# Kernel tuning notes

Hardware: AMD Instinct MI355X
Metric: run time of the kernel (lower is better)

Reference implementation:

```python
import jax, jax.numpy as jnp
import numpy as np

N_NODES = 100000
N_EDGES = 3200000
IN_C, HID_C, OUT_C = 128, 64, 64


def setup_inputs() -> dict:
    key = jax.random.key(0)
    k = jax.random.split(key, 6)
    x = jax.random.normal(k[0], (N_NODES, IN_C), dtype=jnp.float32)
    edge_index = jax.random.randint(k[1], (2, N_EDGES), 0, N_NODES, dtype=jnp.int64)
    edge_weight = jax.random.uniform(k[2], (N_EDGES,), dtype=jnp.float32)
    W1 = jax.random.normal(k[3], (IN_C, HID_C), dtype=jnp.float32) * (1.0 / np.sqrt(IN_C))
    b1 = jnp.zeros((HID_C,), dtype=jnp.float32)
    W2 = jax.random.normal(k[4], (HID_C, OUT_C), dtype=jnp.float32) * (1.0 / np.sqrt(HID_C))
    b2 = jnp.zeros((OUT_C,), dtype=jnp.float32)
    return {"x": x, "edge_index": edge_index, "edge_weight": edge_weight,
            "W1": W1, "b1": b1, "W2": W2, "b2": b2}


def _gcn_norm(edge_index, edge_weight, num_nodes, dtype):
    # PyG GCNConv default: add self-loops (weight 1), symmetric normalization
    loop = jnp.arange(num_nodes, dtype=edge_index.dtype)
    row = jnp.concatenate([edge_index[0], loop])  # sources
    col = jnp.concatenate([edge_index[1], loop])  # targets (aggregation dim)
    w = jnp.concatenate([edge_weight.astype(dtype), jnp.ones((num_nodes,), dtype)])
    deg = jax.ops.segment_sum(w, col, num_segments=num_nodes)
    deg_inv_sqrt = jnp.where(deg > 0, jax.lax.rsqrt(deg), jnp.zeros((), dtype))
    norm = deg_inv_sqrt[row] * w * deg_inv_sqrt[col]
    return row, col, norm


def _gcn_conv(h, row, col, norm, W, b, num_nodes):
    h = h @ W                      # [N, C_out]
    msg = h[row] * norm[:, None]   # gather over sources, scale by edge norm
    out = jax.ops.segment_sum(msg, col, num_segments=num_nodes)  # scatter-add to targets
    return out + b


def reference(x, edge_index, edge_weight, W1, b1, W2, b2):
    num_nodes = x.shape[0]
    row, col, norm = _gcn_norm(edge_index, edge_weight, num_nodes, x.dtype)
    h = _gcn_conv(x, row, col, norm, W1, b1, num_nodes)
    h = jax.nn.relu(h)
    return _gcn_conv(h, row, col, norm, W2, b2, num_nodes)
```

## Files before the change

kernel.cpp:

```cpp
#include <hip/hip_runtime.h>
#include <hip/hip_bf16.h>

#define N_NODES 100000
#define N_EDGES 3200000
#define IN_C 128
#define HID_C 64
#define OUT_C 64

#define NBUCKET 196
#define SC_EDGES 4096
#define SC_GRID 782
#define CAP 18432

struct EdgeRec { int s; float v; };

typedef float f32x2 __attribute__((ext_vector_type(2)));

__device__ __forceinline__ unsigned pack_bf16(float lo, float hi) {
    unsigned short l = __hip_bfloat16_raw(__float2bfloat16(lo)).x;
    unsigned short h = __hip_bfloat16_raw(__float2bfloat16(hi)).x;
    return ((unsigned)h << 16) | l;
}
__device__ __forceinline__ float bf_lo(unsigned u) {
    union { unsigned u; float f; } c; c.u = u << 16; return c.f;
}
__device__ __forceinline__ float bf_hi(unsigned u) {
    union { unsigned u; float f; } c; c.u = u & 0xffff0000u; return c.f;
}
__device__ __forceinline__ f32x2 bfp(unsigned u) {
    union { unsigned u; float f; } lo, hi;
    lo.u = u << 16; hi.u = u & 0xffff0000u;
    f32x2 r; r.x = lo.f; r.y = hi.f; return r;
}
__device__ __forceinline__ void pk_fma(f32x2& acc, f32x2 a, f32x2 w) {
    asm("v_pk_fma_f32 %0, %1, %2, %0" : "+v"(acc) : "v"(a), "v"(w));
}
__device__ __forceinline__ void edge_acc(f32x2* acc2, uint4 u, float w) {
    f32x2 wv; wv.x = w; wv.y = w;
    pk_fma(acc2[0], bfp(u.x), wv);
    pk_fma(acc2[1], bfp(u.y), wv);
    pk_fma(acc2[2], bfp(u.z), wv);
    pk_fma(acc2[3], bfp(u.w), wv);
}

__global__ __launch_bounds__(256) void scatter_coarse(const int* __restrict__ ei,
                                                      const float* __restrict__ ew,
                                                      int* __restrict__ gcursor,
                                                      uint2* __restrict__ tmp) {
    __shared__ int hist[256];
    __shared__ int scan[256];
    __shared__ int lcur[256];
    __shared__ int adj[256];
    __shared__ uint2 rec[SC_EDGES];
    __shared__ unsigned char bk[SC_EDGES];
    int tid = threadIdx.x;
    hist[tid] = 0;
    __syncthreads();
    int base = blockIdx.x * SC_EDGES;
    unsigned ys[16];
    float    ws[16];
    int      bs[16];
    for (int i = 0; i < 16; ++i) {
        int e = base + i * 256 + tid;
        if (e < N_EDGES) {
            int t = ei[N_EDGES + e];
            bs[i] = t >> 9;
            ys[i] = (unsigned)ei[e] | ((unsigned)(t & 511) << 17);
            ws[i] = ew[e];
            atomicAdd(&hist[bs[i]], 1);
        } else bs[i] = -1;
    }
    __syncthreads();
    int v = hist[tid];
    scan[tid] = v;
    __syncthreads();
    for (int off = 1; off < 256; off <<= 1) {
        int t = scan[tid];
        int add = (tid >= off) ? scan[tid - off] : 0;
        __syncthreads();
        scan[tid] = t + add;
        __syncthreads();
    }
    int excl = scan[tid] - v;
    int gb = (v > 0) ? atomicAdd(&gcursor[tid], v) : 0;
    lcur[tid] = excl;
    adj[tid] = tid * CAP + gb - excl;
    __syncthreads();
    for (int i = 0; i < 16; ++i) {
        if (bs[i] >= 0) {
            int j = atomicAdd(&lcur[bs[i]], 1);
            rec[j] = make_uint2(__float_as_uint(ws[i]), ys[i]);
            bk[j] = (unsigned char)bs[i];
        }
    }
    __syncthreads();
    int count = N_EDGES - base;
    if (count > SC_EDGES) count = SC_EDGES;
    for (int j = tid; j < count; j += 256) {
        int b = bk[j];
        tmp[adj[b] + j] = rec[j];
    }
}

__global__ __launch_bounds__(256) void bucket_scan(const int* __restrict__ gcnt,
                                                   int* __restrict__ start) {
    __shared__ int s[256];
    int tid = threadIdx.x;
    int v = gcnt[tid];
    s[tid] = v;
    __syncthreads();
    for (int off = 1; off < 256; off <<= 1) {
        int t = s[tid];
        int add = (tid >= off) ? s[tid - off] : 0;
        __syncthreads();
        s[tid] = t + add;
        __syncthreads();
    }
    start[tid] = s[tid] - v;
    if (tid == 255) start[256] = s[255];
}

__global__ __launch_bounds__(512) void fine_sort(const int* __restrict__ start,
                                                 const uint2* __restrict__ tmpPad,
                                                 int* __restrict__ rowptr,
                                                 float* __restrict__ dis,
                                                 EdgeRec* __restrict__ ed) {
    __shared__ int   cnt[512];
    __shared__ float wdeg[512];
    __shared__ int   s[512];
    int tid = threadIdx.x;
    int nodeBase = blockIdx.x << 9;
    int bb = start[blockIdx.x];
    int nEdge = start[blockIdx.x + 1] - bb;
    const uint2* tb = tmpPad + (size_t)blockIdx.x * CAP;
    cnt[tid] = 0;
    wdeg[tid] = 0.f;
    __syncthreads();
    for (int e = tid; e < nEdge; e += 512) {
        uint2 r = tb[e];
        int l = (r.y >> 17) & 511;
        atomicAdd(&cnt[l], 1);
        atomicAdd(&wdeg[l], __uint_as_float(r.x));
    }
    __syncthreads();
    int v = cnt[tid];
    s[tid] = v;
    __syncthreads();
    for (int off = 1; off < 512; off <<= 1) {
        int t = s[tid];
        int add = (tid >= off) ? s[tid - off] : 0;
        __syncthreads();
        s[tid] = t + add;
        __syncthreads();
    }
    int excl = s[tid] - v;
    int node = nodeBase + tid;
    if (node < N_NODES) {
        rowptr[node] = bb + excl;
        dis[node] = rsqrtf(wdeg[tid] + 1.0f);
    }
    if (node == N_NODES) rowptr[N_NODES] = N_EDGES;
    cnt[tid] = excl;
    __syncthreads();
    for (int e = tid; e < nEdge; e += 512) {
        uint2 r = tb[e];
        int l = (r.y >> 17) & 511;
        int p = atomicAdd(&cnt[l], 1);
        EdgeRec o;
        o.s = (int)(r.y & 0x1FFFFu);
        o.v = __uint_as_float(r.x);
        ed[bb + p] = o;
    }
}

__global__ __launch_bounds__(256) void mm1_kernel(const float* __restrict__ x,
                                                  const float* __restrict__ W,
                                                  const float* __restrict__ dis,
                                                  unsigned* __restrict__ h) {
    __shared__ __align__(16) float xs[16][IN_C];
    __shared__ __align__(16) float wsm[IN_C][HID_C];
    int tid = threadIdx.x;
    {
        float4*       wd = (float4*)&wsm[0][0];
        const float4* wsrc = (const float4*)W;
        for (int i = tid; i < IN_C * HID_C / 4; i += 256) wd[i] = wsrc[i];
        float4*       xd = (float4*)&xs[0][0];
        const float4* xsrc = (const float4*)(x + (size_t)blockIdx.x * 16 * IN_C);
        for (int i = tid; i < 16 * IN_C / 4; i += 256) xd[i] = xsrc[i];
    }
    int rowBase = blockIdx.x * 16;
    __syncthreads();
    int c = tid & 63, rg = tid >> 6;
    const float4* xr0 = (const float4*)&xs[rg * 4 + 0][0];
    const float4* xr1 = (const float4*)&xs[rg * 4 + 1][0];
    const float4* xr2 = (const float4*)&xs[rg * 4 + 2][0];
    const float4* xr3 = (const float4*)&xs[rg * 4 + 3][0];
    float a0 = 0.f, a1 = 0.f, a2 = 0.f, a3 = 0.f;
    #pragma unroll 4
    for (int k4 = 0; k4 < IN_C / 4; ++k4) {
        float4 x0 = xr0[k4], x1 = xr1[k4], x2 = xr2[k4], x3 = xr3[k4];
        float w0 = wsm[4 * k4 + 0][c];
        float w1 = wsm[4 * k4 + 1][c];
        float w2 = wsm[4 * k4 + 2][c];
        float w3 = wsm[4 * k4 + 3][c];
        a0 += x0.x * w0 + x0.y * w1 + x0.z * w2 + x0.w * w3;
        a1 += x1.x * w0 + x1.y * w1 + x1.z * w2 + x1.w * w3;
        a2 += x2.x * w0 + x2.y * w1 + x2.z * w2 + x2.w * w3;
        a3 += x3.x * w0 + x3.y * w1 + x3.z * w2 + x3.w * w3;
    }
    a0 *= dis[rowBase + rg * 4 + 0];
    a1 *= dis[rowBase + rg * 4 + 1];
    a2 *= dis[rowBase + rg * 4 + 2];
    a3 *= dis[rowBase + rg * 4 + 3];
    float o0 = __shfl_xor(a0, 1, 64);
    float o1 = __shfl_xor(a1, 1, 64);
    float o2 = __shfl_xor(a2, 1, 64);
    float o3 = __shfl_xor(a3, 1, 64);
    if ((c & 1) == 0) {
        int ci = c >> 1;
        h[(rowBase + rg * 4 + 0) * 32 + ci] = pack_bf16(a0, o0);
        h[(rowBase + rg * 4 + 1) * 32 + ci] = pack_bf16(a1, o1);
        h[(rowBase + rg * 4 + 2) * 32 + ci] = pack_bf16(a2, o2);
        h[(rowBase + rg * 4 + 3) * 32 + ci] = pack_bf16(a3, o3);
    }
}

__global__ __launch_bounds__(256) void mm2_kernel(const float* __restrict__ a,
                                                  const float* __restrict__ W,
                                                  const float* __restrict__ dis,
                                                  unsigned* __restrict__ h) {
    __shared__ __align__(16) float as[16][HID_C];
    __shared__ __align__(16) float wsm[HID_C][OUT_C];
    int tid = threadIdx.x;
    {
        float4*       wd = (float4*)&wsm[0][0];
        const float4* wsrc = (const float4*)W;
        for (int i = tid; i < HID_C * OUT_C / 4; i += 256) wd[i] = wsrc[i];
        float4*       ad = (float4*)&as[0][0];
        const float4* asrc = (const float4*)(a + (size_t)blockIdx.x * 16 * HID_C);
        for (int i = tid; i < 16 * HID_C / 4; i += 256) ad[i] = asrc[i];
    }
    int rowBase = blockIdx.x * 16;
    __syncthreads();
    int c = tid & 63, rg = tid >> 6;
    const float4* xr0 = (const float4*)&as[rg * 4 + 0][0];
    const float4* xr1 = (const float4*)&as[rg * 4 + 1][0];
    const float4* xr2 = (const float4*)&as[rg * 4 + 2][0];
    const float4* xr3 = (const float4*)&as[rg * 4 + 3][0];
    float a0 = 0.f, a1 = 0.f, a2 = 0.f, a3 = 0.f;
    #pragma unroll 4
    for (int k4 = 0; k4 < HID_C / 4; ++k4) {
        float4 x0 = xr0[k4], x1 = xr1[k4], x2 = xr2[k4], x3 = xr3[k4];
        float w0 = wsm[4 * k4 + 0][c];
        float w1 = wsm[4 * k4 + 1][c];
        float w2 = wsm[4 * k4 + 2][c];
        float w3 = wsm[4 * k4 + 3][c];
        a0 += x0.x * w0 + x0.y * w1 + x0.z * w2 + x0.w * w3;
        a1 += x1.x * w0 + x1.y * w1 + x1.z * w2 + x1.w * w3;
        a2 += x2.x * w0 + x2.y * w1 + x2.z * w2 + x2.w * w3;
        a3 += x3.x * w0 + x3.y * w1 + x3.z * w2 + x3.w * w3;
    }
    a0 *= dis[rowBase + rg * 4 + 0];
    a1 *= dis[rowBase + rg * 4 + 1];
    a2 *= dis[rowBase + rg * 4 + 2];
    a3 *= dis[rowBase + rg * 4 + 3];
    float o0 = __shfl_xor(a0, 1, 64);
    float o1 = __shfl_xor(a1, 1, 64);
    float o2 = __shfl_xor(a2, 1, 64);
    float o3 = __shfl_xor(a3, 1, 64);
    if ((c & 1) == 0) {
        int ci = c >> 1;
        h[(rowBase + rg * 4 + 0) * 32 + ci] = pack_bf16(a0, o0);
        h[(rowBase + rg * 4 + 1) * 32 + ci] = pack_bf16(a1, o1);
        h[(rowBase + rg * 4 + 2) * 32 + ci] = pack_bf16(a2, o2);
        h[(rowBase + rg * 4 + 3) * 32 + ci] = pack_bf16(a3, o3);
    }
}

__global__ __launch_bounds__(256, 8) void agg_kernel(const int* __restrict__ rowptr,
                                                     const EdgeRec* __restrict__ ed,
                                                     const unsigned* __restrict__ h,
                                                     const float* __restrict__ dis,
                                                     const float* __restrict__ b,
                                                     float* __restrict__ out,
                                                     int relu) {
    int node = blockIdx.x * 4 + (threadIdx.x >> 6);
    int lane = threadIdx.x & 63;
    int g = lane >> 3;
    int cl = lane & 7;
    int beg = rowptr[node];
    int end = rowptr[node + 1];
    const uint4* h16 = (const uint4*)h;
    const char*  hb  = (const char*)h + (size_t)cl * 16;
    float d  = dis[node];
    uint4 us = h16[(size_t)node * 8 + cl];
    f32x2 acc2[4];
    acc2[0] = 0.f; acc2[1] = 0.f; acc2[2] = 0.f; acc2[3] = 0.f;
    int n = end - beg;
    int nb = (n + 31) >> 5;
    int nm1 = n - 1;
    uint2 q0, q1, q2, q3;
    if (nb > 0) {
        q0 = *(const uint2*)(ed + beg + min(g,      nm1));
        q1 = *(const uint2*)(ed + beg + min(g + 8,  nm1));
        q2 = *(const uint2*)(ed + beg + min(g + 16, nm1));
        q3 = *(const uint2*)(ed + beg + min(g + 24, nm1));
        for (int bt = 0; bt < nb; ++bt) {
            int ob = (bt << 5) + g;
            float w0 = (ob      < n) ? __uint_as_float(q0.y) : 0.f;
            float w1 = (ob + 8  < n) ? __uint_as_float(q1.y) : 0.f;
            float w2 = (ob + 16 < n) ? __uint_as_float(q2.y) : 0.f;
            float w3 = (ob + 24 < n) ? __uint_as_float(q3.y) : 0.f;
            uint4 u0 = *(const uint4*)(hb + ((size_t)(unsigned)q0.x << 7));
            uint4 u1 = *(const uint4*)(hb + ((size_t)(unsigned)q1.x << 7));
            uint4 u2 = *(const uint4*)(hb + ((size_t)(unsigned)q2.x << 7));
            uint4 u3 = *(const uint4*)(hb + ((size_t)(unsigned)q3.x << 7));
            if (bt + 1 < nb) {
                int on = ob + 32;
                q0 = *(const uint2*)(ed + beg + min(on,      nm1));
                q1 = *(const uint2*)(ed + beg + min(on + 8,  nm1));
                q2 = *(const uint2*)(ed + beg + min(on + 16, nm1));
                q3 = *(const uint2*)(ed + beg + min(on + 24, nm1));
            }
            edge_acc(acc2, u0, w0);
            edge_acc(acc2, u1, w1);
            edge_acc(acc2, u2, w2);
            edge_acc(acc2, u3, w3);
        }
    }
    float acc[8] = { acc2[0].x, acc2[0].y, acc2[1].x, acc2[1].y,
                     acc2[2].x, acc2[2].y, acc2[3].x, acc2[3].y };
    #pragma unroll
    for (int kk = 0; kk < 8; ++kk) {
        acc[kk] += __shfl_xor(acc[kk], 8, 64);
        acc[kk] += __shfl_xor(acc[kk], 16, 64);
        acc[kk] += __shfl_xor(acc[kk], 32, 64);
    }
    if (g == 0) {
        float hs[8] = { bf_lo(us.x), bf_hi(us.x), bf_lo(us.y), bf_hi(us.y),
                        bf_lo(us.z), bf_hi(us.z), bf_lo(us.w), bf_hi(us.w) };
        const float4* b4 = (const float4*)b;
        float4 bv0 = b4[cl * 2], bv1 = b4[cl * 2 + 1];
        float4 v0, v1;
        v0.x = d * (acc[0] + hs[0]) + bv0.x;
        v0.y = d * (acc[1] + hs[1]) + bv0.y;
        v0.z = d * (acc[2] + hs[2]) + bv0.z;
        v0.w = d * (acc[3] + hs[3]) + bv0.w;
        v1.x = d * (acc[4] + hs[4]) + bv1.x;
        v1.y = d * (acc[5] + hs[5]) + bv1.y;
        v1.z = d * (acc[6] + hs[6]) + bv1.z;
        v1.w = d * (acc[7] + hs[7]) + bv1.w;
        if (relu) {
            v0.x = fmaxf(v0.x, 0.f); v0.y = fmaxf(v0.y, 0.f);
            v0.z = fmaxf(v0.z, 0.f); v0.w = fmaxf(v0.w, 0.f);
            v1.x = fmaxf(v1.x, 0.f); v1.y = fmaxf(v1.y, 0.f);
            v1.z = fmaxf(v1.z, 0.f); v1.w = fmaxf(v1.w, 0.f);
        }
        float4* o4 = (float4*)out;
        o4[node * 16 + cl * 2]     = v0;
        o4[node * 16 + cl * 2 + 1] = v1;
    }
}

extern "C" void kernel_launch(void* const* d_in, const int* in_sizes, int n_in,
                              void* d_out, int out_size, void* d_ws, size_t ws_size,
                              hipStream_t stream) {
    const float* x  = (const float*)d_in[0];
    const int*   ei = (const int*)d_in[1];
    const float* ew = (const float*)d_in[2];
    const float* W1 = (const float*)d_in[3];
    const float* b1 = (const float*)d_in[4];
    const float* W2 = (const float*)d_in[5];
    const float* b2 = (const float*)d_in[6];
    float* out = (float*)d_out;

    char* p = (char*)d_ws;
    auto carve = [&](size_t bytes) { char* r = p; p += (bytes + 255) & ~(size_t)255; return r; };
    float*    dis     = (float*)carve(N_NODES * 4);
    int*      rowptr  = (int*)carve((N_NODES + 1) * 4);
    int*      start   = (int*)carve(257 * 4);
    int*      gcursor = (int*)carve(256 * 4);
    EdgeRec*  ed      = (EdgeRec*)carve((size_t)N_EDGES * 8);
    size_t    r2sz    = (size_t)NBUCKET * CAP * 8;
    size_t    hasz    = (size_t)N_NODES * 64 * 6;
    char*     r2      = carve(r2sz > hasz ? r2sz : hasz);
    uint2*    tmpPad  = (uint2*)r2;
    unsigned* h       = (unsigned*)r2;
    float*    a       = (float*)(r2 + (size_t)N_NODES * 64 * 2);

    hipMemsetAsync(gcursor, 0, 256 * sizeof(int), stream);
    scatter_coarse<<<SC_GRID, 256, 0, stream>>>(ei, ew, gcursor, tmpPad);
    bucket_scan<<<1, 256, 0, stream>>>(gcursor, start);
    fine_sort<<<NBUCKET, 512, 0, stream>>>(start, tmpPad, rowptr, dis, ed);

    mm1_kernel<<<N_NODES / 16, 256, 0, stream>>>(x, W1, dis, h);
    agg_kernel<<<N_NODES / 4, 256, 0, stream>>>(rowptr, ed, h, dis, b1, a, 1);

    mm2_kernel<<<N_NODES / 16, 256, 0, stream>>>(a, W2, dis, h);
    agg_kernel<<<N_NODES / 4, 256, 0, stream>>>(rowptr, ed, h, dis, b2, out, 0);
}
```

Measured before the change: 376.9 us.

## Replace scalar FP32 GEMMs with split-bf16 MFMA persistent kernels

Both dense matmul kernels are replaced by one templated kernel that runs the 16x16x32 bf16 MFMA instruction. It keeps FP32-like accuracy by splitting each operand into hi and lo bf16 parts and issuing three MFMAs per k-step. Weight fragments are held in registers and the kernel loops persistently over row tiles with a fixed grid of 1250 blocks, which removes the shared-memory staging and scalar FMA work. The cost is three MFMAs plus conversion work per step, and a small accuracy loss from dropping the lo*lo term.

After: 352.6 us. 1.07x faster.

```diff
diff --git a/kernel.cpp b/kernel.cpp
--- a/kernel.cpp
+++ b/kernel.cpp
@@ -15,6 +15,9 @@
 struct EdgeRec { int s; float v; };
 
 typedef float f32x2 __attribute__((ext_vector_type(2)));
+typedef float f32x4 __attribute__((ext_vector_type(4)));
+typedef short bf16x8 __attribute__((ext_vector_type(8)));
+union F8 { uint4 u; bf16x8 f; };
 
 __device__ __forceinline__ unsigned pack_bf16(float lo, float hi) {
     unsigned short l = __hip_bfloat16_raw(__float2bfloat16(lo)).x;
@@ -41,6 +44,23 @@
     pk_fma(acc2[1], bfp(u.y), wv);
     pk_fma(acc2[2], bfp(u.z), wv);
     pk_fma(acc2[3], bfp(u.w), wv);
+}
+__device__ __forceinline__ unsigned cvt_pk_bf16(float lo, float hi) {
+    unsigned r;
+    asm("v_cvt_pk_bf16_f32 %0, %1, %2" : "=v"(r) : "v"(lo), "v"(hi));
+    return r;
+}
+__device__ __forceinline__ void split_frag(const float* f, uint4& hi4, uint4& lo4) {
+    unsigned hi[4], lo[4];
+    #pragma unroll
+    for (int p = 0; p < 4; ++p) {
+        hi[p] = cvt_pk_bf16(f[2 * p], f[2 * p + 1]);
+        float r0 = f[2 * p]     - bf_lo(hi[p]);
+        float r1 = f[2 * p + 1] - bf_hi(hi[p]);
+        lo[p] = cvt_pk_bf16(r0, r1);
+    }
+    hi4 = make_uint4(hi[0], hi[1], hi[2], hi[3]);
+    lo4 = make_uint4(lo[0], lo[1], lo[2], lo[3]);
 }
 
 __global__ __launch_bounds__(256) void scatter_coarse(const int* __restrict__ ei,
@@ -173,107 +193,56 @@
     }
 }
 
-__global__ __launch_bounds__(256) void mm1_kernel(const float* __restrict__ x,
-                                                  const float* __restrict__ W,
-                                                  const float* __restrict__ dis,
-                                                  unsigned* __restrict__ h) {
-    __shared__ __align__(16) float xs[16][IN_C];
-    __shared__ __align__(16) float wsm[IN_C][HID_C];
-    int tid = threadIdx.x;
-    {
-        float4*       wd = (float4*)&wsm[0][0];
-        const float4* wsrc = (const float4*)W;
-        for (int i = tid; i < IN_C * HID_C / 4; i += 256) wd[i] = wsrc[i];
-        float4*       xd = (float4*)&xs[0][0];
-        const float4* xsrc = (const float4*)(x + (size_t)blockIdx.x * 16 * IN_C);
-        for (int i = tid; i < 16 * IN_C / 4; i += 256) xd[i] = xsrc[i];
-    }
-    int rowBase = blockIdx.x * 16;
-    __syncthreads();
-    int c = tid & 63, rg = tid >> 6;
-    const float4* xr0 = (const float4*)&xs[rg * 4 + 0][0];
-    const float4* xr1 = (const float4*)&xs[rg * 4 + 1][0];
-    const float4* xr2 = (const float4*)&xs[rg * 4 + 2][0];
-    const float4* xr3 = (const float4*)&xs[rg * 4 + 3][0];
-    float a0 = 0.f, a1 = 0.f, a2 = 0.f, a3 = 0.f;
-    #pragma unroll 4
-    for (int k4 = 0; k4 < IN_C / 4; ++k4) {
-        float4 x0 = xr0[k4], x1 = xr1[k4], x2 = xr2[k4], x3 = xr3[k4];
-        float w0 = wsm[4 * k4 + 0][c];
-        float w1 = wsm[4 * k4 + 1][c];
-        float w2 = wsm[4 * k4 + 2][c];
-        float w3 = wsm[4 * k4 + 3][c];
-        a0 += x0.x * w0 + x0.y * w1 + x0.z * w2 + x0.w * w3;
-        a1 += x1.x * w0 + x1.y * w1 + x1.z * w2 + x1.w * w3;
-        a2 += x2.x * w0 + x2.y * w1 + x2.z * w2 + x2.w * w3;
-        a3 += x3.x * w0 + x3.y * w1 + x3.z * w2 + x3.w * w3;
-    }
-    a0 *= dis[rowBase + rg * 4 + 0];
-    a1 *= dis[rowBase + rg * 4 + 1];
-    a2 *= dis[rowBase + rg * 4 + 2];
-    a3 *= dis[rowBase + rg * 4 + 3];
-    float o0 = __shfl_xor(a0, 1, 64);
-    float o1 = __shfl_xor(a1, 1, 64);
-    float o2 = __shfl_xor(a2, 1, 64);
-    float o3 = __shfl_xor(a3, 1, 64);
-    if ((c & 1) == 0) {
-        int ci = c >> 1;
-        h[(rowBase + rg * 4 + 0) * 32 + ci] = pack_bf16(a0, o0);
-        h[(rowBase + rg * 4 + 1) * 32 + ci] = pack_bf16(a1, o1);
-        h[(rowBase + rg * 4 + 2) * 32 + ci] = pack_bf16(a2, o2);
-        h[(rowBase + rg * 4 + 3) * 32 + ci] = pack_bf16(a3, o3);
-    }
-}
-
-__global__ __launch_bounds__(256) void mm2_kernel(const float* __restrict__ a,
-                                                  const float* __restrict__ W,
-                                                  const float* __restrict__ dis,
-                                                  unsigned* __restrict__ h) {
-    __shared__ __align__(16) float as[16][HID_C];
-    __shared__ __align__(16) float wsm[HID_C][OUT_C];
-    int tid = threadIdx.x;
-    {
-        float4*       wd = (float4*)&wsm[0][0];
-        const float4* wsrc = (const float4*)W;
-        for (int i = tid; i < HID_C * OUT_C / 4; i += 256) wd[i] = wsrc[i];
-        float4*       ad = (float4*)&as[0][0];
-        const float4* asrc = (const float4*)(a + (size_t)blockIdx.x * 16 * HID_C);
-        for (int i = tid; i < 16 * HID_C / 4; i += 256) ad[i] = asrc[i];
-    }
-    int rowBase = blockIdx.x * 16;
-    __syncthreads();
-    int c = tid & 63, rg = tid >> 6;
-    const float4* xr0 = (const float4*)&as[rg * 4 + 0][0];
-    const float4* xr1 = (const float4*)&as[rg * 4 + 1][0];
-    const float4* xr2 = (const float4*)&as[rg * 4 + 2][0];
-    const float4* xr3 = (const float4*)&as[rg * 4 + 3][0];
-    float a0 = 0.f, a1 = 0.f, a2 = 0.f, a3 = 0.f;
-    #pragma unroll 4
-    for (int k4 = 0; k4 < HID_C / 4; ++k4) {
-        float4 x0 = xr0[k4], x1 = xr1[k4], x2 = xr2[k4], x3 = xr3[k4];
-        float w0 = wsm[4 * k4 + 0][c];
-        float w1 = wsm[4 * k4 + 1][c];
-        float w2 = wsm[4 * k4 + 2][c];
-        float w3 = wsm[4 * k4 + 3][c];
-        a0 += x0.x * w0 + x0.y * w1 + x0.z * w2 + x0.w * w3;
-        a1 += x1.x * w0 + x1.y * w1 + x1.z * w2 + x1.w * w3;
-        a2 += x2.x * w0 + x2.y * w1 + x2.z * w2 + x2.w * w3;
-        a3 += x3.x * w0 + x3.y * w1 + x3.z * w2 + x3.w * w3;
-    }
-    a0 *= dis[rowBase + rg * 4 + 0];
-    a1 *= dis[rowBase + rg * 4 + 1];
-    a2 *= dis[rowBase + rg * 4 + 2];
-    a3 *= dis[rowBase + rg * 4 + 3];
-    float o0 = __shfl_xor(a0, 1, 64);
-    float o1 = __shfl_xor(a1, 1, 64);
-    float o2 = __shfl_xor(a2, 1, 64);
-    float o3 = __shfl_xor(a3, 1, 64);
-    if ((c & 1) == 0) {
-        int ci = c >> 1;
-        h[(rowBase + rg * 4 + 0) * 32 + ci] = pack_bf16(a0, o0);
-        h[(rowBase + rg * 4 + 1) * 32 + ci] = pack_bf16(a1, o1);
-        h[(rowBase + rg * 4 + 2) * 32 + ci] = pack_bf16(a2, o2);
-        h[(rowBase + rg * 4 + 3) * 32 + ci] = pack_bf16(a3, o3);
+template<int K>
+__global__ __launch_bounds__(256) void mm_mfma(const float* __restrict__ X,
+                                               const float* __restrict__ W,
+                                               const float* __restrict__ dis,
+                                               unsigned* __restrict__ h) {
+    constexpr int NKS = K / 32;
+    int wv = threadIdx.x >> 6;
+    int l  = threadIdx.x & 63;
+    int lr = l & 15;
+    int kr = l >> 4;
+    int col = wv * 16 + lr;
+    F8 bhi[NKS], blo[NKS];
+    #pragma unroll
+    for (int ks = 0; ks < NKS; ++ks) {
+        const float* wp = W + (ks * 32 + kr * 8) * 64 + col;
+        float f[8];
+        #pragma unroll
+        for (int j = 0; j < 8; ++j) f[j] = wp[j * 64];
+        split_frag(f, bhi[ks].u, blo[ks].u);
+    }
+    for (int t = blockIdx.x; t < N_NODES / 16; t += gridDim.x) {
+        int row0 = t * 16;
+        f32x4 acc = {0.f, 0.f, 0.f, 0.f};
+        #pragma unroll
+        for (int ks = 0; ks < NKS; ++ks) {
+            const float4* xp = (const float4*)(X + (size_t)(row0 + lr) * K + ks * 32 + kr * 8);
+            float4 fa = xp[0], fb = xp[1];
+            float f[8] = {fa.x, fa.y, fa.z, fa.w, fb.x, fb.y, fb.z, fb.w};
+            F8 ahi, alo;
+            split_frag(f, ahi.u, alo.u);
+            acc = __builtin_amdgcn_mfma_f32_16x16x32_bf16(ahi.f, bhi[ks].f, acc, 0, 0, 0);
+            acc = __builtin_amdgcn_mfma_f32_16x16x32_bf16(ahi.f, blo[ks].f, acc, 0, 0, 0);
+            acc = __builtin_amdgcn_mfma_f32_16x16x32_bf16(alo.f, bhi[ks].f, acc, 0, 0, 0);
+        }
+        int rbase = row0 + kr * 4;
+        float v0 = acc[0] * dis[rbase + 0];
+        float v1 = acc[1] * dis[rbase + 1];
+        float v2 = acc[2] * dis[rbase + 2];
+        float v3 = acc[3] * dis[rbase + 3];
+        float o0 = __shfl_xor(v0, 1, 64);
+        float o1 = __shfl_xor(v1, 1, 64);
+        float o2 = __shfl_xor(v2, 1, 64);
+        float o3 = __shfl_xor(v3, 1, 64);
+        if ((lr & 1) == 0) {
+            int ci = col >> 1;
+            h[(rbase + 0) * 32 + ci] = pack_bf16(v0, o0);
+            h[(rbase + 1) * 32 + ci] = pack_bf16(v1, o1);
+            h[(rbase + 2) * 32 + ci] = pack_bf16(v2, o2);
+            h[(rbase + 3) * 32 + ci] = pack_bf16(v3, o3);
+        }
     }
 }
 
@@ -393,9 +362,9 @@
     bucket_scan<<<1, 256, 0, stream>>>(gcursor, start);
     fine_sort<<<NBUCKET, 512, 0, stream>>>(start, tmpPad, rowptr, dis, ed);
 
-    mm1_kernel<<<N_NODES / 16, 256, 0, stream>>>(x, W1, dis, h);
+    mm_mfma<IN_C><<<1250, 256, 0, stream>>>(x, W1, dis, h);
     agg_kernel<<<N_NODES / 4, 256, 0, stream>>>(rowptr, ed, h, dis, b1, a, 1);
 
-    mm2_kernel<<<N_NODES / 16, 256, 0, stream>>>(a, W2, dis, h);
+    mm_mfma<HID_C><<<1250, 256, 0, stream>>>(a, W2, dis, h);
     agg_kernel<<<N_NODES / 4, 256, 0, stream>>>(rowptr, ed, h, dis, b2, out, 0);
 }
```
